# Performance work log

Hardware: AMD Instinct MI355X
Metric: run time of the kernel (lower is better)

## Reference

```python
import jax, jax.numpy as jnp
import numpy as np

N_NODES = 100000
N_EDGES = 1600000
IN_F = 256
OUT_F = 128


def setup_inputs() -> dict:
    key = jax.random.key(0)
    k1, k2, k3, k4, k5, k6 = jax.random.split(key, 6)
    X_input = jax.random.normal(k1, (N_NODES, IN_F), dtype=jnp.float32)
    adj_row = jax.random.randint(k2, (N_EDGES,), 0, N_NODES, dtype=jnp.int32)
    adj_col = jax.random.randint(k3, (N_EDGES,), 0, N_NODES, dtype=jnp.int32)
    adj_val = jax.random.uniform(k4, (N_EDGES,), dtype=jnp.float32)
    W = jax.random.normal(k5, (IN_F, OUT_F), dtype=jnp.float32) / np.sqrt(IN_F)
    bias = jax.random.normal(k6, (OUT_F,), dtype=jnp.float32) * 0.01
    return {"X_input": X_input, "adj_row": adj_row, "adj_col": adj_col,
            "adj_val": adj_val, "W": W, "bias": bias}


def reference(X_input, adj_row, adj_col, adj_val, W, bias):
    # dense linear (no bias): support = X @ W   [N, out]
    support = X_input @ W
    # sparse adjacency matmul (COO spmm): out[r] += val * support[c]
    messages = adj_val[:, None] * support[adj_col]          # [E, out]
    output = jax.ops.segment_sum(messages, adj_row, num_segments=N_NODES)
    return output + bias
```

## Files before the change

### kernel.cpp

```cpp
#include <hip/hip_runtime.h>

#define N_NODES 100000
#define N_EDGES 1600000
#define IN_F    256
#define OUT_F   128

#define BROWS2   256
#define NB2      391
#define CAPB     4800
#define PART_EPB 4096
#define KE       (PART_EPB / 256)
#define KB       ((CAPB + 255) / 256)

typedef __attribute__((ext_vector_type(8))) short   s16x8;
typedef __attribute__((ext_vector_type(4))) float   f32x4;
typedef __attribute__((ext_vector_type(8))) unsigned short u16x8;

__device__ __forceinline__ unsigned short f2bf(float f) {
    unsigned u = __float_as_uint(f);
    u += 0x7FFFu + ((u >> 16) & 1u);
    return (unsigned short)(u >> 16);
}
__device__ __forceinline__ float bf2f(unsigned short h) {
    return __uint_as_float((unsigned)h << 16);
}

__global__ __launch_bounds__(256) void wt_build(const float* __restrict__ W,
                                                unsigned short* __restrict__ Wt,
                                                int* __restrict__ cursorA) {
    const int n = blockIdx.x;
    const int k = threadIdx.x;
    Wt[n * IN_F + k] = f2bf(W[(size_t)k * OUT_F + n]);
    const int idx = blockIdx.x * 256 + threadIdx.x;
    if (idx < NB2) cursorA[idx] = 0;
}

__global__ __launch_bounds__(256) void gemm_mfma(const float* __restrict__ X,
                                                 const unsigned short* __restrict__ Wt,
                                                 unsigned short* __restrict__ support) {
    __shared__ unsigned short As[64][40];
    __shared__ unsigned short Bs[128][40];
    __shared__ unsigned short Ct[64][136];

    const int t    = threadIdx.x;
    const int wid  = t >> 6;
    const int lane = t & 63;
    const int tm   = lane & 15;
    const int quad = lane >> 4;
    const int row0 = blockIdx.x * 64;

    f32x4 acc[8];
#pragma unroll
    for (int c = 0; c < 8; ++c) acc[c] = (f32x4){0.f, 0.f, 0.f, 0.f};

    for (int kb = 0; kb < IN_F; kb += 32) {
        {
            const int m  = t >> 2;
            const int k0 = (t & 3) * 8;
            const int gr = row0 + m;
            float4 x0 = make_float4(0.f, 0.f, 0.f, 0.f), x1 = x0;
            if (gr < N_NODES) {
                const float* xp = &X[(size_t)gr * IN_F + kb + k0];
                x0 = *(const float4*)xp;
                x1 = *(const float4*)(xp + 4);
            }
            ushort4 a0, a1;
            a0.x = f2bf(x0.x); a0.y = f2bf(x0.y); a0.z = f2bf(x0.z); a0.w = f2bf(x0.w);
            a1.x = f2bf(x1.x); a1.y = f2bf(x1.y); a1.z = f2bf(x1.z); a1.w = f2bf(x1.w);
            *(ushort4*)&As[m][k0]     = a0;
            *(ushort4*)&As[m][k0 + 4] = a1;
        }
        {
            const int n  = t >> 1;
            const int k0 = (t & 1) * 16;
            const unsigned short* wp = &Wt[(size_t)n * IN_F + kb + k0];
            *(u16x8*)&Bs[n][k0]     = *(const u16x8*)wp;
            *(u16x8*)&Bs[n][k0 + 8] = *(const u16x8*)(wp + 8);
        }
        __syncthreads();

        const s16x8 a = *(const s16x8*)&As[wid * 16 + tm][quad * 8];
#pragma unroll
        for (int c = 0; c < 8; ++c) {
            const s16x8 b = *(const s16x8*)&Bs[c * 16 + tm][quad * 8];
            acc[c] = __builtin_amdgcn_mfma_f32_16x16x32_bf16(a, b, acc[c], 0, 0, 0);
        }
        __syncthreads();
    }

#pragma unroll
    for (int c = 0; c < 8; ++c) {
        const int col = c * 16 + tm;
#pragma unroll
        for (int reg = 0; reg < 4; ++reg) {
            const int m = wid * 16 + quad * 4 + reg;
            Ct[m][col] = f2bf(acc[c][reg]);
        }
    }
    __syncthreads();
    {
        const int m   = t >> 2;
        const int seg = (t & 3) * 32;
        const int gr  = row0 + m;
        if (gr < N_NODES) {
            unsigned short* op = &support[(size_t)gr * OUT_F + seg];
#pragma unroll
            for (int i = 0; i < 4; ++i)
                *(u16x8*)(op + i * 8) = *(const u16x8*)&Ct[m][seg + i * 8];
        }
    }
}

__global__ __launch_bounds__(256) void partition_edges(const int* __restrict__ arow,
                                                       const int* __restrict__ acol,
                                                       const float* __restrict__ aval,
                                                       int* __restrict__ cursorA,
                                                       int2* __restrict__ epackA) {
    __shared__ int cnt[NB2];
    __shared__ int basep[NB2];
    const int t = threadIdx.x;
    for (int k = t; k < NB2; k += 256) cnt[k] = 0;
    __syncthreads();

    const int base = blockIdx.x * PART_EPB;
    int pk_[KE], vv_[KE], b_[KE], rk_[KE];
#pragma unroll
    for (int k = 0; k < KE; ++k) {
        const int i = base + t + k * 256;
        b_[k] = -1;
        if (i < N_EDGES) {
            const int r = arow[i];
            b_[k]  = r >> 8;
            pk_[k] = ((r & (BROWS2 - 1)) << 17) | acol[i];
            vv_[k] = __float_as_int(aval[i]);
            rk_[k] = atomicAdd(&cnt[b_[k]], 1);
        }
    }
    __syncthreads();
    for (int k = t; k < NB2; k += 256) {
        const int c = cnt[k];
        if (c > 0) basep[k] = atomicAdd(&cursorA[k], c);
    }
    __syncthreads();
#pragma unroll
    for (int k = 0; k < KE; ++k) {
        if (b_[k] >= 0) {
            const int pos = basep[b_[k]] + rk_[k];
            if (pos < CAPB)
                epackA[(size_t)b_[k] * CAPB + pos] = make_int2(pk_[k], vv_[k]);
        }
    }
}

__global__ __launch_bounds__(256) void bucket_build(const int* __restrict__ cursorA,
                                                    const int2* __restrict__ epackA,
                                                    int2* __restrict__ rowmeta,
                                                    int2* __restrict__ epackB) {
    __shared__ int cnt[BROWS2];
    __shared__ int excl[BROWS2];
    __shared__ int wsum[4];
    const int b = blockIdx.x;
    const int t = threadIdx.x;
    cnt[t] = 0;
    __syncthreads();

    const size_t sa = (size_t)b * CAPB;
    const int n = min(cursorA[b], CAPB);

    int pk_[KB], vv_[KB], rk_[KB];
#pragma unroll
    for (int k = 0; k < KB; ++k) {
        const int i = t + k * 256;
        rk_[k] = -1;
        if (i < n) {
            const int2 e = epackA[sa + i];
            pk_[k] = e.x;
            vv_[k] = e.y;
            rk_[k] = atomicAdd(&cnt[e.x >> 17], 1);
        }
    }
    __syncthreads();

    {
        const int lane = t & 63;
        const int my   = cnt[t];
        int x = my;
#pragma unroll
        for (int off = 1; off < 64; off <<= 1) {
            const int y = __shfl_up(x, off, 64);
            if (lane >= off) x += y;
        }
        if (lane == 63) wsum[t >> 6] = x;
        __syncthreads();
        int pre = x - my;
        const int w = t >> 6;
        for (int kk = 0; kk < w; ++kk) pre += wsum[kk];
        excl[t] = pre;
        const int r = b * BROWS2 + t;
        if (r < N_NODES) rowmeta[r] = make_int2((int)sa + pre, my);
    }
    __syncthreads();

#pragma unroll
    for (int k = 0; k < KB; ++k) {
        if (rk_[k] >= 0) {
            const int rl  = pk_[k] >> 17;
            const int pos = excl[rl] + rk_[k];
            epackB[sa + pos] = make_int2(pk_[k] & 0x1FFFF, vv_[k]);
        }
    }
}

__global__ __launch_bounds__(256) void csr_gather(const int2* __restrict__ rowmeta,
                                                  const int2* __restrict__ epackB,
                                                  const unsigned short* __restrict__ support,
                                                  const float* __restrict__ bias,
                                                  float* __restrict__ out) {
    const int t = threadIdx.x;
    const int g = t >> 5;
    const int l = t & 31;
    const int r = blockIdx.x * 8 + g;
    if (r >= N_NODES) return;

    const int2 rm   = rowmeta[r];
    const int start = rm.x;
    const int deg   = rm.y;

    float4 acc = *(const float4*)&bias[l * 4];

    int i = 0;
    for (; i + 4 <= deg; i += 4) {
        const int2 e0 = epackB[start + i + 0];
        const int2 e1 = epackB[start + i + 1];
        const int2 e2 = epackB[start + i + 2];
        const int2 e3 = epackB[start + i + 3];
        const ushort4 u0 = *(const ushort4*)&support[(size_t)e0.x * OUT_F + l * 4];
        const ushort4 u1 = *(const ushort4*)&support[(size_t)e1.x * OUT_F + l * 4];
        const ushort4 u2 = *(const ushort4*)&support[(size_t)e2.x * OUT_F + l * 4];
        const ushort4 u3 = *(const ushort4*)&support[(size_t)e3.x * OUT_F + l * 4];
        const float v0 = __int_as_float(e0.y);
        const float v1 = __int_as_float(e1.y);
        const float v2 = __int_as_float(e2.y);
        const float v3 = __int_as_float(e3.y);
        acc.x = fmaf(v0, bf2f(u0.x), fmaf(v1, bf2f(u1.x), fmaf(v2, bf2f(u2.x), fmaf(v3, bf2f(u3.x), acc.x))));
        acc.y = fmaf(v0, bf2f(u0.y), fmaf(v1, bf2f(u1.y), fmaf(v2, bf2f(u2.y), fmaf(v3, bf2f(u3.y), acc.y))));
        acc.z = fmaf(v0, bf2f(u0.z), fmaf(v1, bf2f(u1.z), fmaf(v2, bf2f(u2.z), fmaf(v3, bf2f(u3.z), acc.z))));
        acc.w = fmaf(v0, bf2f(u0.w), fmaf(v1, bf2f(u1.w), fmaf(v2, bf2f(u2.w), fmaf(v3, bf2f(u3.w), acc.w))));
    }
    for (; i < deg; ++i) {
        const int2 e = epackB[start + i];
        const ushort4 u = *(const ushort4*)&support[(size_t)e.x * OUT_F + l * 4];
        const float v = __int_as_float(e.y);
        acc.x = fmaf(v, bf2f(u.x), acc.x);
        acc.y = fmaf(v, bf2f(u.y), acc.y);
        acc.z = fmaf(v, bf2f(u.z), acc.z);
        acc.w = fmaf(v, bf2f(u.w), acc.w);
    }

    *(float4*)&out[(size_t)r * OUT_F + l * 4] = acc;
}

extern "C" void kernel_launch(void* const* d_in, const int* in_sizes, int n_in,
                              void* d_out, int out_size, void* d_ws, size_t ws_size,
                              hipStream_t stream) {
    const float* X    = (const float*)d_in[0];
    const int*   arow = (const int*)d_in[1];
    const int*   acol = (const int*)d_in[2];
    const float* aval = (const float*)d_in[3];
    const float* W    = (const float*)d_in[4];
    const float* bias = (const float*)d_in[5];
    float*       out  = (float*)d_out;

    char* ws = (char*)d_ws;
    unsigned short* support = (unsigned short*)ws;  ws += (size_t)N_NODES * OUT_F * 2;
    unsigned short* Wt = (unsigned short*)ws;       ws += (size_t)IN_F * OUT_F * 2;
    int2* rowmeta = (int2*)ws;                      ws += (size_t)N_NODES * 8;
    int*  cursorA = (int*)ws;                       ws += ((NB2 + 7) & ~7) * 4;
    int2* epackB  = (int2*)ws;
    int2* epackA  = (int2*)d_out;

    wt_build<<<OUT_F, 256, 0, stream>>>(W, Wt, cursorA);
    gemm_mfma<<<(N_NODES + 63) / 64, 256, 0, stream>>>(X, Wt, support);
    partition_edges<<<(N_EDGES + PART_EPB - 1) / PART_EPB, 256, 0, stream>>>(
        arow, acol, aval, cursorA, epackA);
    bucket_build<<<NB2, 256, 0, stream>>>(cursorA, epackA, rowmeta, epackB);
    csr_gather<<<(N_NODES + 7) / 8, 256, 0, stream>>>(
        rowmeta, epackB, support, bias, out);
}
```

Before: 289.4 us.

## Fuse GEMM and edge partition into one launch, widen bucket build, unroll gather

Merges the bf16 MFMA GEMM and the edge partitioning kernel into one launch that splits work by block index, with a shared-memory union, so the two independent stages can run on the GPU at the same time. Partition blocks now take 2048 edges each. The bucket build kernel moves to 512 threads per block with fewer elements per thread, and the CSR gather loop is unrolled to 8 edges so more loads are in flight. This trades a larger combined grid and more register pressure in the gather for fewer launches and better overlap.

```diff
diff --git a/kernel.cpp b/kernel.cpp
--- a/kernel.cpp
+++ b/kernel.cpp
@@ -8,9 +8,11 @@
 #define BROWS2   256
 #define NB2      391
 #define CAPB     4800
-#define PART_EPB 4096
+#define PART_EPB 2048
+#define NPART    782
 #define KE       (PART_EPB / 256)
-#define KB       ((CAPB + 255) / 256)
+#define NGEMM    1563
+#define KB       ((CAPB + 511) / 512)
 
 typedef __attribute__((ext_vector_type(8))) short   s16x8;
 typedef __attribute__((ext_vector_type(4))) float   f32x4;
@@ -35,19 +37,68 @@
     if (idx < NB2) cursorA[idx] = 0;
 }
 
-__global__ __launch_bounds__(256) void gemm_mfma(const float* __restrict__ X,
-                                                 const unsigned short* __restrict__ Wt,
-                                                 unsigned short* __restrict__ support) {
-    __shared__ unsigned short As[64][40];
-    __shared__ unsigned short Bs[128][40];
-    __shared__ unsigned short Ct[64][136];
-
-    const int t    = threadIdx.x;
+__global__ __launch_bounds__(256) void fused_gp(const float* __restrict__ X,
+                                                const unsigned short* __restrict__ Wt,
+                                                unsigned short* __restrict__ support,
+                                                const int* __restrict__ arow,
+                                                const int* __restrict__ acol,
+                                                const float* __restrict__ aval,
+                                                int* __restrict__ cursorA,
+                                                int2* __restrict__ epackA) {
+    __shared__ union {
+        struct {
+            unsigned short As[64][40];
+            unsigned short Bs[128][40];
+            unsigned short Ct[64][136];
+        } g;
+        struct {
+            int cnt[NB2];
+            int basep[NB2];
+        } p;
+    } sm;
+
+    const int t = threadIdx.x;
+
+    if (blockIdx.x < NPART) {
+        for (int k = t; k < NB2; k += 256) sm.p.cnt[k] = 0;
+        __syncthreads();
+
+        const int base = blockIdx.x * PART_EPB;
+        int pk_[KE], vv_[KE], b_[KE], rk_[KE];
+#pragma unroll
+        for (int k = 0; k < KE; ++k) {
+            const int i = base + t + k * 256;
+            b_[k] = -1;
+            if (i < N_EDGES) {
+                const int r = arow[i];
+                b_[k]  = r >> 8;
+                pk_[k] = ((r & (BROWS2 - 1)) << 17) | acol[i];
+                vv_[k] = __float_as_int(aval[i]);
+                rk_[k] = atomicAdd(&sm.p.cnt[b_[k]], 1);
+            }
+        }
+        __syncthreads();
+        for (int k = t; k < NB2; k += 256) {
+            const int c = sm.p.cnt[k];
+            if (c > 0) sm.p.basep[k] = atomicAdd(&cursorA[k], c);
+        }
+        __syncthreads();
+#pragma unroll
+        for (int k = 0; k < KE; ++k) {
+            if (b_[k] >= 0) {
+                const int pos = sm.p.basep[b_[k]] + rk_[k];
+                if (pos < CAPB)
+                    epackA[(size_t)b_[k] * CAPB + pos] = make_int2(pk_[k], vv_[k]);
+            }
+        }
+        return;
+    }
+
     const int wid  = t >> 6;
     const int lane = t & 63;
     const int tm   = lane & 15;
     const int quad = lane >> 4;
-    const int row0 = blockIdx.x * 64;
+    const int row0 = (blockIdx.x - NPART) * 64;
 
     f32x4 acc[8];
 #pragma unroll
@@ -67,22 +118,22 @@
             ushort4 a0, a1;
             a0.x = f2bf(x0.x); a0.y = f2bf(x0.y); a0.z = f2bf(x0.z); a0.w = f2bf(x0.w);
             a1.x = f2bf(x1.x); a1.y = f2bf(x1.y); a1.z = f2bf(x1.z); a1.w = f2bf(x1.w);
-            *(ushort4*)&As[m][k0]     = a0;
-            *(ushort4*)&As[m][k0 + 4] = a1;
+            *(ushort4*)&sm.g.As[m][k0]     = a0;
+            *(ushort4*)&sm.g.As[m][k0 + 4] = a1;
         }
         {
             const int n  = t >> 1;
             const int k0 = (t & 1) * 16;
             const unsigned short* wp = &Wt[(size_t)n * IN_F + kb + k0];
-            *(u16x8*)&Bs[n][k0]     = *(const u16x8*)wp;
-            *(u16x8*)&Bs[n][k0 + 8] = *(const u16x8*)(wp + 8);
-        }
-        __syncthreads();
-
-        const s16x8 a = *(const s16x8*)&As[wid * 16 + tm][quad * 8];
+            *(u16x8*)&sm.g.Bs[n][k0]     = *(const u16x8*)wp;
+            *(u16x8*)&sm.g.Bs[n][k0 + 8] = *(const u16x8*)(wp + 8);
+        }
+        __syncthreads();
+
+        const s16x8 a = *(const s16x8*)&sm.g.As[wid * 16 + tm][quad * 8];
 #pragma unroll
         for (int c = 0; c < 8; ++c) {
-            const s16x8 b = *(const s16x8*)&Bs[c * 16 + tm][quad * 8];
+            const s16x8 b = *(const s16x8*)&sm.g.Bs[c * 16 + tm][quad * 8];
             acc[c] = __builtin_amdgcn_mfma_f32_16x16x32_bf16(a, b, acc[c], 0, 0, 0);
         }
         __syncthreads();
@@ -94,7 +145,7 @@
 #pragma unroll
         for (int reg = 0; reg < 4; ++reg) {
             const int m = wid * 16 + quad * 4 + reg;
-            Ct[m][col] = f2bf(acc[c][reg]);
+            sm.g.Ct[m][col] = f2bf(acc[c][reg]);
         }
     }
     __syncthreads();
@@ -106,53 +157,12 @@
             unsigned short* op = &support[(size_t)gr * OUT_F + seg];
 #pragma unroll
             for (int i = 0; i < 4; ++i)
-                *(u16x8*)(op + i * 8) = *(const u16x8*)&Ct[m][seg + i * 8];
-        }
-    }
-}
-
-__global__ __launch_bounds__(256) void partition_edges(const int* __restrict__ arow,
-                                                       const int* __restrict__ acol,
-                                                       const float* __restrict__ aval,
-                                                       int* __restrict__ cursorA,
-                                                       int2* __restrict__ epackA) {
-    __shared__ int cnt[NB2];
-    __shared__ int basep[NB2];
-    const int t = threadIdx.x;
-    for (int k = t; k < NB2; k += 256) cnt[k] = 0;
-    __syncthreads();
-
-    const int base = blockIdx.x * PART_EPB;
-    int pk_[KE], vv_[KE], b_[KE], rk_[KE];
-#pragma unroll
-    for (int k = 0; k < KE; ++k) {
-        const int i = base + t + k * 256;
-        b_[k] = -1;
-        if (i < N_EDGES) {
-            const int r = arow[i];
-            b_[k]  = r >> 8;
-            pk_[k] = ((r & (BROWS2 - 1)) << 17) | acol[i];
-            vv_[k] = __float_as_int(aval[i]);
-            rk_[k] = atomicAdd(&cnt[b_[k]], 1);
-        }
-    }
-    __syncthreads();
-    for (int k = t; k < NB2; k += 256) {
-        const int c = cnt[k];
-        if (c > 0) basep[k] = atomicAdd(&cursorA[k], c);
-    }
-    __syncthreads();
-#pragma unroll
-    for (int k = 0; k < KE; ++k) {
-        if (b_[k] >= 0) {
-            const int pos = basep[b_[k]] + rk_[k];
-            if (pos < CAPB)
-                epackA[(size_t)b_[k] * CAPB + pos] = make_int2(pk_[k], vv_[k]);
-        }
-    }
-}
-
-__global__ __launch_bounds__(256) void bucket_build(const int* __restrict__ cursorA,
+                *(u16x8*)(op + i * 8) = *(const u16x8*)&sm.g.Ct[m][seg + i * 8];
+        }
+    }
+}
+
+__global__ __launch_bounds__(512) void bucket_build(const int* __restrict__ cursorA,
                                                     const int2* __restrict__ epackA,
                                                     int2* __restrict__ rowmeta,
                                                     int2* __restrict__ epackB) {
@@ -161,7 +171,7 @@
     __shared__ int wsum[4];
     const int b = blockIdx.x;
     const int t = threadIdx.x;
-    cnt[t] = 0;
+    if (t < BROWS2) cnt[t] = 0;
     __syncthreads();
 
     const size_t sa = (size_t)b * CAPB;
@@ -170,7 +180,7 @@
     int pk_[KB], vv_[KB], rk_[KB];
 #pragma unroll
     for (int k = 0; k < KB; ++k) {
-        const int i = t + k * 256;
+        const int i = t + k * 512;
         rk_[k] = -1;
         if (i < n) {
             const int2 e = epackA[sa + i];
@@ -181,17 +191,20 @@
     }
     __syncthreads();
 
-    {
+    int x = 0, my = 0;
+    if (t < BROWS2) {
         const int lane = t & 63;
-        const int my   = cnt[t];
-        int x = my;
+        my = cnt[t];
+        x  = my;
 #pragma unroll
         for (int off = 1; off < 64; off <<= 1) {
             const int y = __shfl_up(x, off, 64);
             if (lane >= off) x += y;
         }
         if (lane == 63) wsum[t >> 6] = x;
-        __syncthreads();
+    }
+    __syncthreads();
+    if (t < BROWS2) {
         int pre = x - my;
         const int w = t >> 6;
         for (int kk = 0; kk < w; ++kk) pre += wsum[kk];
@@ -229,6 +242,36 @@
     float4 acc = *(const float4*)&bias[l * 4];
 
     int i = 0;
+    for (; i + 8 <= deg; i += 8) {
+        const int2 e0 = epackB[start + i + 0];
+        const int2 e1 = epackB[start + i + 1];
+        const int2 e2 = epackB[start + i + 2];
+        const int2 e3 = epackB[start + i + 3];
+        const int2 e4 = epackB[start + i + 4];
+        const int2 e5 = epackB[start + i + 5];
+        const int2 e6 = epackB[start + i + 6];
+        const int2 e7 = epackB[start + i + 7];
+        const ushort4 u0 = *(const ushort4*)&support[(size_t)e0.x * OUT_F + l * 4];
+        const ushort4 u1 = *(const ushort4*)&support[(size_t)e1.x * OUT_F + l * 4];
+        const ushort4 u2 = *(const ushort4*)&support[(size_t)e2.x * OUT_F + l * 4];
+        const ushort4 u3 = *(const ushort4*)&support[(size_t)e3.x * OUT_F + l * 4];
+        const ushort4 u4 = *(const ushort4*)&support[(size_t)e4.x * OUT_F + l * 4];
+        const ushort4 u5 = *(const ushort4*)&support[(size_t)e5.x * OUT_F + l * 4];
+        const ushort4 u6 = *(const ushort4*)&support[(size_t)e6.x * OUT_F + l * 4];
+        const ushort4 u7 = *(const ushort4*)&support[(size_t)e7.x * OUT_F + l * 4];
+        const float v0 = __int_as_float(e0.y), v1 = __int_as_float(e1.y);
+        const float v2 = __int_as_float(e2.y), v3 = __int_as_float(e3.y);
+        const float v4 = __int_as_float(e4.y), v5 = __int_as_float(e5.y);
+        const float v6 = __int_as_float(e6.y), v7 = __int_as_float(e7.y);
+        acc.x = fmaf(v0, bf2f(u0.x), fmaf(v1, bf2f(u1.x), fmaf(v2, bf2f(u2.x), fmaf(v3, bf2f(u3.x), acc.x))));
+        acc.y = fmaf(v0, bf2f(u0.y), fmaf(v1, bf2f(u1.y), fmaf(v2, bf2f(u2.y), fmaf(v3, bf2f(u3.y), acc.y))));
+        acc.z = fmaf(v0, bf2f(u0.z), fmaf(v1, bf2f(u1.z), fmaf(v2, bf2f(u2.z), fmaf(v3, bf2f(u3.z), acc.z))));
+        acc.w = fmaf(v0, bf2f(u0.w), fmaf(v1, bf2f(u1.w), fmaf(v2, bf2f(u2.w), fmaf(v3, bf2f(u3.w), acc.w))));
+        acc.x = fmaf(v4, bf2f(u4.x), fmaf(v5, bf2f(u5.x), fmaf(v6, bf2f(u6.x), fmaf(v7, bf2f(u7.x), acc.x))));
+        acc.y = fmaf(v4, bf2f(u4.y), fmaf(v5, bf2f(u5.y), fmaf(v6, bf2f(u6.y), fmaf(v7, bf2f(u7.y), acc.y))));
+        acc.z = fmaf(v4, bf2f(u4.z), fmaf(v5, bf2f(u5.z), fmaf(v6, bf2f(u6.z), fmaf(v7, bf2f(u7.z), acc.z))));
+        acc.w = fmaf(v4, bf2f(u4.w), fmaf(v5, bf2f(u5.w), fmaf(v6, bf2f(u6.w), fmaf(v7, bf2f(u7.w), acc.w))));
+    }
     for (; i + 4 <= deg; i += 4) {
         const int2 e0 = epackB[start + i + 0];
         const int2 e1 = epackB[start + i + 1];
@@ -238,10 +281,8 @@
         const ushort4 u1 = *(const ushort4*)&support[(size_t)e1.x * OUT_F + l * 4];
         const ushort4 u2 = *(const ushort4*)&support[(size_t)e2.x * OUT_F + l * 4];
         const ushort4 u3 = *(const ushort4*)&support[(size_t)e3.x * OUT_F + l * 4];
-        const float v0 = __int_as_float(e0.y);
-        const float v1 = __int_as_float(e1.y);
-        const float v2 = __int_as_float(e2.y);
-        const float v3 = __int_as_float(e3.y);
+        const float v0 = __int_as_float(e0.y), v1 = __int_as_float(e1.y);
+        const float v2 = __int_as_float(e2.y), v3 = __int_as_float(e3.y);
         acc.x = fmaf(v0, bf2f(u0.x), fmaf(v1, bf2f(u1.x), fmaf(v2, bf2f(u2.x), fmaf(v3, bf2f(u3.x), acc.x))));
         acc.y = fmaf(v0, bf2f(u0.y), fmaf(v1, bf2f(u1.y), fmaf(v2, bf2f(u2.y), fmaf(v3, bf2f(u3.y), acc.y))));
         acc.z = fmaf(v0, bf2f(u0.z), fmaf(v1, bf2f(u1.z), fmaf(v2, bf2f(u2.z), fmaf(v3, bf2f(u3.z), acc.z))));
@@ -280,10 +321,9 @@
     int2* epackA  = (int2*)d_out;
 
     wt_build<<<OUT_F, 256, 0, stream>>>(W, Wt, cursorA);
-    gemm_mfma<<<(N_NODES + 63) / 64, 256, 0, stream>>>(X, Wt, support);
-    partition_edges<<<(N_EDGES + PART_EPB - 1) / PART_EPB, 256, 0, stream>>>(
-        arow, acol, aval, cursorA, epackA);
-    bucket_build<<<NB2, 256, 0, stream>>>(cursorA, epackA, rowmeta, epackB);
+    fused_gp<<<NPART + NGEMM, 256, 0, stream>>>(X, Wt, support,
+                                                arow, acol, aval, cursorA, epackA);
+    bucket_build<<<NB2, 512, 0, stream>>>(cursorA, epackA, rowmeta, epackB);
     csr_gather<<<(N_NODES + 7) / 8, 256, 0, stream>>>(
         rowmeta, epackB, support, bias, out);
 }
```

After: 307.9 us. 6.4% more time.

## Fuse weight prep, GEMM, partition and bucket build into one cooperative kernel

Applied to the files above, without the earlier changes.

Merges the four preprocessing kernels into a single persistent cooperative kernel that uses grid-wide syncs between phases and a union of shared-memory layouts. The goal is to remove per-launch overhead and inter-kernel gaps. The grid is sized from occupancy, and the code falls back to the separate kernels if the cooperative launch fails. The risks are slower grid.sync barriers, and lower occupancy because the shared-memory union is sized for the GEMM phase, which could make the GEMM and scatter phases slower than in their dedicated kernels.

```diff
diff --git a/kernel.cpp b/kernel.cpp
--- a/kernel.cpp
+++ b/kernel.cpp
@@ -1,4 +1,7 @@
 #include <hip/hip_runtime.h>
+#include <hip/hip_cooperative_groups.h>
+
+namespace cg = cooperative_groups;
 
 #define N_NODES 100000
 #define N_EDGES 1600000
@@ -9,8 +12,10 @@
 #define NB2      391
 #define CAPB     4800
 #define PART_EPB 4096
+#define NPARTC   391
 #define KE       (PART_EPB / 256)
 #define KB       ((CAPB + 255) / 256)
+#define NGEMM    1563
 
 typedef __attribute__((ext_vector_type(8))) short   s16x8;
 typedef __attribute__((ext_vector_type(4))) float   f32x4;
@@ -23,6 +28,197 @@
 }
 __device__ __forceinline__ float bf2f(unsigned short h) {
     return __uint_as_float((unsigned)h << 16);
+}
+
+struct SmG {
+    unsigned short As[64][40];
+    unsigned short Bs[128][40];
+    unsigned short Ct[64][136];
+};
+struct SmP { int cnt[NB2]; int basep[NB2]; };
+struct SmB { int cnt[BROWS2]; int excl[BROWS2]; int wsum[4]; };
+
+__global__ __launch_bounds__(256) void mega(const float* __restrict__ X,
+                                            const int* __restrict__ arow,
+                                            const int* __restrict__ acol,
+                                            const float* __restrict__ aval,
+                                            const float* __restrict__ W,
+                                            unsigned short* __restrict__ support,
+                                            unsigned short* __restrict__ Wt,
+                                            int* __restrict__ cursorA,
+                                            int2* __restrict__ epackA,
+                                            int2* __restrict__ rowmeta,
+                                            int2* __restrict__ epackB) {
+    __shared__ union { SmG g; SmP p; SmB b; } sm;
+    cg::grid_group grid = cg::this_grid();
+    const int t   = threadIdx.x;
+    const int bid = blockIdx.x;
+    const int nb  = gridDim.x;
+
+    for (int n = bid; n < OUT_F; n += nb)
+        Wt[n * IN_F + t] = f2bf(W[(size_t)t * OUT_F + n]);
+    if (bid == 0)
+        for (int k = t; k < NB2; k += 256) cursorA[k] = 0;
+    grid.sync();
+
+    for (int c = bid; c < NPARTC; c += nb) {
+        for (int k = t; k < NB2; k += 256) sm.p.cnt[k] = 0;
+        __syncthreads();
+
+        const int base = c * PART_EPB;
+        int pk_[KE], vv_[KE], b_[KE], rk_[KE];
+#pragma unroll
+        for (int k = 0; k < KE; ++k) {
+            const int i = base + t + k * 256;
+            b_[k] = -1;
+            if (i < N_EDGES) {
+                const int r = arow[i];
+                b_[k]  = r >> 8;
+                pk_[k] = ((r & (BROWS2 - 1)) << 17) | acol[i];
+                vv_[k] = __float_as_int(aval[i]);
+                rk_[k] = atomicAdd(&sm.p.cnt[b_[k]], 1);
+            }
+        }
+        __syncthreads();
+        for (int k = t; k < NB2; k += 256) {
+            const int cc = sm.p.cnt[k];
+            if (cc > 0) sm.p.basep[k] = atomicAdd(&cursorA[k], cc);
+        }
+        __syncthreads();
+#pragma unroll
+        for (int k = 0; k < KE; ++k) {
+            if (b_[k] >= 0) {
+                const int pos = sm.p.basep[b_[k]] + rk_[k];
+                if (pos < CAPB)
+                    epackA[(size_t)b_[k] * CAPB + pos] = make_int2(pk_[k], vv_[k]);
+            }
+        }
+        __syncthreads();
+    }
+    grid.sync();
+
+    for (int tile = bid; tile < NGEMM; tile += nb) {
+        const int wid  = t >> 6;
+        const int lane = t & 63;
+        const int tm   = lane & 15;
+        const int quad = lane >> 4;
+        const int row0 = tile * 64;
+
+        f32x4 acc[8];
+#pragma unroll
+        for (int c = 0; c < 8; ++c) acc[c] = (f32x4){0.f, 0.f, 0.f, 0.f};
+
+        for (int kb = 0; kb < IN_F; kb += 32) {
+            {
+                const int m  = t >> 2;
+                const int k0 = (t & 3) * 8;
+                const int gr = row0 + m;
+                float4 x0 = make_float4(0.f, 0.f, 0.f, 0.f), x1 = x0;
+                if (gr < N_NODES) {
+                    const float* xp = &X[(size_t)gr * IN_F + kb + k0];
+                    x0 = *(const float4*)xp;
+                    x1 = *(const float4*)(xp + 4);
+                }
+                ushort4 a0, a1;
+                a0.x = f2bf(x0.x); a0.y = f2bf(x0.y); a0.z = f2bf(x0.z); a0.w = f2bf(x0.w);
+                a1.x = f2bf(x1.x); a1.y = f2bf(x1.y); a1.z = f2bf(x1.z); a1.w = f2bf(x1.w);
+                *(ushort4*)&sm.g.As[m][k0]     = a0;
+                *(ushort4*)&sm.g.As[m][k0 + 4] = a1;
+            }
+            {
+                const int n  = t >> 1;
+                const int k0 = (t & 1) * 16;
+                const unsigned short* wp = &Wt[(size_t)n * IN_F + kb + k0];
+                *(u16x8*)&sm.g.Bs[n][k0]     = *(const u16x8*)wp;
+                *(u16x8*)&sm.g.Bs[n][k0 + 8] = *(const u16x8*)(wp + 8);
+            }
+            __syncthreads();
+
+            const s16x8 a = *(const s16x8*)&sm.g.As[wid * 16 + tm][quad * 8];
+#pragma unroll
+            for (int c = 0; c < 8; ++c) {
+                const s16x8 b = *(const s16x8*)&sm.g.Bs[c * 16 + tm][quad * 8];
+                acc[c] = __builtin_amdgcn_mfma_f32_16x16x32_bf16(a, b, acc[c], 0, 0, 0);
+            }
+            __syncthreads();
+        }
+
+#pragma unroll
+        for (int c = 0; c < 8; ++c) {
+            const int col = c * 16 + tm;
+#pragma unroll
+            for (int reg = 0; reg < 4; ++reg) {
+                const int m = wid * 16 + quad * 4 + reg;
+                sm.g.Ct[m][col] = f2bf(acc[c][reg]);
+            }
+        }
+        __syncthreads();
+        {
+            const int m   = t >> 2;
+            const int seg = (t & 3) * 32;
+            const int gr  = row0 + m;
+            if (gr < N_NODES) {
+                unsigned short* op = &support[(size_t)gr * OUT_F + seg];
+#pragma unroll
+                for (int i = 0; i < 4; ++i)
+                    *(u16x8*)(op + i * 8) = *(const u16x8*)&sm.g.Ct[m][seg + i * 8];
+            }
+        }
+        __syncthreads();
+    }
+    grid.sync();
+
+    for (int b = bid; b < NB2; b += nb) {
+        sm.b.cnt[t] = 0;
+        __syncthreads();
+
+        const size_t sa = (size_t)b * CAPB;
+        const int n = min(cursorA[b], CAPB);
+
+        int pk_[KB], vv_[KB], rk_[KB];
+#pragma unroll
+        for (int k = 0; k < KB; ++k) {
+            const int i = t + k * 256;
+            rk_[k] = -1;
+            if (i < n) {
+                const int2 e = epackA[sa + i];
+                pk_[k] = e.x;
+                vv_[k] = e.y;
+                rk_[k] = atomicAdd(&sm.b.cnt[e.x >> 17], 1);
+            }
+        }
+        __syncthreads();
+
+        {
+            const int lane = t & 63;
+            const int my   = sm.b.cnt[t];
+            int x = my;
+#pragma unroll
+            for (int off = 1; off < 64; off <<= 1) {
+                const int y = __shfl_up(x, off, 64);
+                if (lane >= off) x += y;
+            }
+            if (lane == 63) sm.b.wsum[t >> 6] = x;
+            __syncthreads();
+            int pre = x - my;
+            const int w = t >> 6;
+            for (int kk = 0; kk < w; ++kk) pre += sm.b.wsum[kk];
+            sm.b.excl[t] = pre;
+            const int r = b * BROWS2 + t;
+            if (r < N_NODES) rowmeta[r] = make_int2((int)sa + pre, my);
+        }
+        __syncthreads();
+
+#pragma unroll
+        for (int k = 0; k < KB; ++k) {
+            if (rk_[k] >= 0) {
+                const int rl  = pk_[k] >> 17;
+                const int pos = sm.b.excl[rl] + rk_[k];
+                epackB[sa + pos] = make_int2(pk_[k] & 0x1FFFF, vv_[k]);
+            }
+        }
+        __syncthreads();
+    }
 }
 
 __global__ __launch_bounds__(256) void wt_build(const float* __restrict__ W,
@@ -279,11 +475,42 @@
     int2* epackB  = (int2*)ws;
     int2* epackA  = (int2*)d_out;
 
-    wt_build<<<OUT_F, 256, 0, stream>>>(W, Wt, cursorA);
-    gemm_mfma<<<(N_NODES + 63) / 64, 256, 0, stream>>>(X, Wt, support);
-    partition_edges<<<(N_EDGES + PART_EPB - 1) / PART_EPB, 256, 0, stream>>>(
-        arow, acol, aval, cursorA, epackA);
-    bucket_build<<<NB2, 256, 0, stream>>>(cursorA, epackA, rowmeta, epackB);
+    static int coopGrid = -1;
+    if (coopGrid == -1) {
+        int perCU = 0, numCU = 0, dev = 0;
+        if (hipGetDevice(&dev) == hipSuccess &&
+            hipOccupancyMaxActiveBlocksPerMultiprocessor(
+                &perCU, (const void*)mega, 256, 0) == hipSuccess && perCU >= 1 &&
+            hipDeviceGetAttribute(&numCU, hipDeviceAttributeMultiprocessorCount,
+                                  dev) == hipSuccess && numCU >= 1) {
+            long g = (long)perCU * numCU;
+            coopGrid = (int)(g > 2048 ? 2048 : g);
+        } else {
+            coopGrid = 0;
+        }
+    }
+
+    bool coopOK = false;
+    if (coopGrid > 0) {
+        void* args[] = {(void*)&X, (void*)&arow, (void*)&acol, (void*)&aval,
+                        (void*)&W, (void*)&support, (void*)&Wt, (void*)&cursorA,
+                        (void*)&epackA, (void*)&rowmeta, (void*)&epackB};
+        if (hipLaunchCooperativeKernel((const void*)mega, dim3(coopGrid),
+                                       dim3(256), args, 0, stream) == hipSuccess) {
+            coopOK = true;
+        } else {
+            (void)hipGetLastError();
+            coopGrid = 0;
+        }
+    }
+
+    if (!coopOK) {
+        wt_build<<<OUT_F, 256, 0, stream>>>(W, Wt, cursorA);
+        gemm_mfma<<<NGEMM, 256, 0, stream>>>(X, Wt, support);
+        partition_edges<<<NPARTC, 256, 0, stream>>>(arow, acol, aval, cursorA, epackA);
+        bucket_build<<<NB2, 256, 0, stream>>>(cursorA, epackA, rowmeta, epackB);
+    }
+
     csr_gather<<<(N_NODES + 7) / 8, 256, 0, stream>>>(
         rowmeta, epackB, support, bias, out);
 }
```

New measurement: 452.1 us. 1.56x slower.

## Load GEMM tiles directly to LDS with swizzled fp32 A and packed bf16 conversion

Applied to the files above, without the earlier changes.

The GEMM now stages X tiles as fp32 and W tiles through global_load_lds direct-to-LDS copies instead of register round-trips. The X layout in LDS is XOR-swizzled, and W is pre-laid out in k-chunk-major order so each copy is a contiguous 1 KB block. The bf16 conversion of A moves to after the LDS read and uses the hardware v_cvt_pk_bf16_f32 instruction. This is meant to cut VGPR staging and conversion ALU work in the load phase, at the cost of twice the LDS bytes for A. It still keeps the single-buffered loop with two barriers per k-step.

```diff
diff --git a/kernel.cpp b/kernel.cpp
--- a/kernel.cpp
+++ b/kernel.cpp
@@ -11,6 +11,7 @@
 #define PART_EPB 4096
 #define KE       (PART_EPB / 256)
 #define KB       ((CAPB + 255) / 256)
+#define NGEMM    1563
 
 typedef __attribute__((ext_vector_type(8))) short   s16x8;
 typedef __attribute__((ext_vector_type(4))) float   f32x4;
@@ -23,6 +24,17 @@
 }
 __device__ __forceinline__ float bf2f(unsigned short h) {
     return __uint_as_float((unsigned)h << 16);
+}
+
+__device__ __forceinline__ void gl_lds16(const void* g, void* l) {
+    __builtin_amdgcn_global_load_lds((const __attribute__((address_space(1))) void*)g,
+                                     (__attribute__((address_space(3))) void*)l,
+                                     16, 0, 0);
+}
+__device__ __forceinline__ unsigned cvt_pk_bf16(float lo, float hi) {
+    unsigned r;
+    asm("v_cvt_pk_bf16_f32 %0, %1, %2" : "=v"(r) : "v"(lo), "v"(hi));
+    return r;
 }
 
 __global__ __launch_bounds__(256) void wt_build(const float* __restrict__ W,
@@ -30,7 +42,7 @@
                                                 int* __restrict__ cursorA) {
     const int n = blockIdx.x;
     const int k = threadIdx.x;
-    Wt[n * IN_F + k] = f2bf(W[(size_t)k * OUT_F + n]);
+    Wt[(k >> 3) * 1024 + n * 8 + (k & 7)] = f2bf(W[(size_t)k * OUT_F + n]);
     const int idx = blockIdx.x * 256 + threadIdx.x;
     if (idx < NB2) cursorA[idx] = 0;
 }
@@ -38,9 +50,10 @@
 __global__ __launch_bounds__(256) void gemm_mfma(const float* __restrict__ X,
                                                  const unsigned short* __restrict__ Wt,
                                                  unsigned short* __restrict__ support) {
-    __shared__ unsigned short As[64][40];
-    __shared__ unsigned short Bs[128][40];
-    __shared__ unsigned short Ct[64][136];
+    __shared__ __align__(16) char smem[17408];
+    unsigned short* Bs  = (unsigned short*)smem;
+    float*          Asf = (float*)(smem + 8192);
+    unsigned short* Ct  = (unsigned short*)smem;
 
     const int t    = threadIdx.x;
     const int wid  = t >> 6;
@@ -49,41 +62,53 @@
     const int quad = lane >> 4;
     const int row0 = blockIdx.x * 64;
 
+    const char* srcA[2];
+    char*       dstA[2];
+#pragma unroll
+    for (int i = 0; i < 2; ++i) {
+        const int s  = wid * 128 + i * 64 + lane;
+        const int r  = s >> 3;
+        const int jj = (s & 7) ^ (r & 7);
+        const int gr = min(row0 + r, N_NODES - 1);
+        srcA[i] = (const char*)X + (size_t)gr * (IN_F * 4) + jj * 16;
+        dstA[i] = (char*)Asf + (size_t)(wid * 128 + i * 64) * 16;
+    }
+    const char* srcB[2];
+    char*       dstB[2];
+#pragma unroll
+    for (int i = 0; i < 2; ++i) {
+        const int c1k = wid * 2 + i;
+        srcB[i] = (const char*)Wt + (size_t)c1k * 1024 + lane * 16;
+        dstB[i] = (char*)Bs + (size_t)c1k * 1024;
+    }
+
     f32x4 acc[8];
 #pragma unroll
     for (int c = 0; c < 8; ++c) acc[c] = (f32x4){0.f, 0.f, 0.f, 0.f};
 
-    for (int kb = 0; kb < IN_F; kb += 32) {
-        {
-            const int m  = t >> 2;
-            const int k0 = (t & 3) * 8;
-            const int gr = row0 + m;
-            float4 x0 = make_float4(0.f, 0.f, 0.f, 0.f), x1 = x0;
-            if (gr < N_NODES) {
-                const float* xp = &X[(size_t)gr * IN_F + kb + k0];
-                x0 = *(const float4*)xp;
-                x1 = *(const float4*)(xp + 4);
-            }
-            ushort4 a0, a1;
-            a0.x = f2bf(x0.x); a0.y = f2bf(x0.y); a0.z = f2bf(x0.z); a0.w = f2bf(x0.w);
-            a1.x = f2bf(x1.x); a1.y = f2bf(x1.y); a1.z = f2bf(x1.z); a1.w = f2bf(x1.w);
-            *(ushort4*)&As[m][k0]     = a0;
-            *(ushort4*)&As[m][k0 + 4] = a1;
-        }
-        {
-            const int n  = t >> 1;
-            const int k0 = (t & 1) * 16;
-            const unsigned short* wp = &Wt[(size_t)n * IN_F + kb + k0];
-            *(u16x8*)&Bs[n][k0]     = *(const u16x8*)wp;
-            *(u16x8*)&Bs[n][k0 + 8] = *(const u16x8*)(wp + 8);
-        }
+    for (int ks = 0; ks < 8; ++ks) {
+        gl_lds16(srcA[0], dstA[0]);
+        gl_lds16(srcA[1], dstA[1]);
+        gl_lds16(srcB[0], dstB[0]);
+        gl_lds16(srcB[1], dstB[1]);
+        srcA[0] += 128; srcA[1] += 128;
+        srcB[0] += 8192; srcB[1] += 8192;
         __syncthreads();
 
-        const s16x8 a = *(const s16x8*)&As[wid * 16 + tm][quad * 8];
+        const int r  = wid * 16 + tm;
+        const int j0 = quad * 2;
+        const float4 a0 = *(const float4*)&Asf[(r * 8 + (j0 ^ (r & 7))) * 4];
+        const float4 a1 = *(const float4*)&Asf[(r * 8 + ((j0 + 1) ^ (r & 7))) * 4];
+        union { s16x8 v; unsigned u[4]; } af;
+        af.u[0] = cvt_pk_bf16(a0.x, a0.y);
+        af.u[1] = cvt_pk_bf16(a0.z, a0.w);
+        af.u[2] = cvt_pk_bf16(a1.x, a1.y);
+        af.u[3] = cvt_pk_bf16(a1.z, a1.w);
+
 #pragma unroll
         for (int c = 0; c < 8; ++c) {
-            const s16x8 b = *(const s16x8*)&Bs[c * 16 + tm][quad * 8];
-            acc[c] = __builtin_amdgcn_mfma_f32_16x16x32_bf16(a, b, acc[c], 0, 0, 0);
+            const s16x8 b = *(const s16x8*)&Bs[(quad * 128 + c * 16 + tm) * 8];
+            acc[c] = __builtin_amdgcn_mfma_f32_16x16x32_bf16(af.v, b, acc[c], 0, 0, 0);
         }
         __syncthreads();
     }
@@ -94,7 +119,7 @@
 #pragma unroll
         for (int reg = 0; reg < 4; ++reg) {
             const int m = wid * 16 + quad * 4 + reg;
-            Ct[m][col] = f2bf(acc[c][reg]);
+            Ct[m * 136 + col] = f2bf(acc[c][reg]);
         }
     }
     __syncthreads();
@@ -106,7 +131,7 @@
             unsigned short* op = &support[(size_t)gr * OUT_F + seg];
 #pragma unroll
             for (int i = 0; i < 4; ++i)
-                *(u16x8*)(op + i * 8) = *(const u16x8*)&Ct[m][seg + i * 8];
+                *(u16x8*)(op + i * 8) = *(const u16x8*)&Ct[m * 136 + seg + i * 8];
         }
     }
 }
@@ -280,7 +305,7 @@
     int2* epackA  = (int2*)d_out;
 
     wt_build<<<OUT_F, 256, 0, stream>>>(W, Wt, cursorA);
-    gemm_mfma<<<(N_NODES + 63) / 64, 256, 0, stream>>>(X, Wt, support);
+    gemm_mfma<<<NGEMM, 256, 0, stream>>>(X, Wt, support);
     partition_edges<<<(N_EDGES + PART_EPB - 1) / PART_EPB, 256, 0, stream>>>(
         arow, acol, aval, cursorA, epackA);
     bucket_build<<<NB2, 256, 0, stream>>>(cursorA, epackA, rowmeta, epackB);
```

Result: no change. 289.7 us (+0.1%).
